# Kernel optimization log

Hardware: AMD Instinct MI355X
Metric: run time of the kernel (lower is better)

The kernel has to match this reference:

```python
import jax, jax.numpy as jnp
import numpy as np

EPS = 1e-5  # PyTorch BatchNorm2d default eps


def _batchnorm(x, gamma, beta):
    # training-mode BN over (N, T, V) per channel; x: [N, C, T, V]
    mean = jnp.mean(x, axis=(0, 2, 3), keepdims=True)
    var = jnp.var(x, axis=(0, 2, 3), keepdims=True)
    inv = jax.lax.rsqrt(var + EPS)
    return (x - mean) * inv * gamma[None, :, None, None] + beta[None, :, None, None]


def setup_inputs() -> dict:
    key = jax.random.key(0)
    ks = jax.random.split(key, 8)
    N, Cin, Cout, T, V, S = 64, 64, 128, 300, 25, 3
    x = jax.random.normal(ks[0], (N, Cin, T, V), dtype=jnp.float32)
    A = jax.random.uniform(ks[1], (S, V, V), dtype=jnp.float32)
    # per-subset 1x1 conv weights/biases (kaiming-ish scale)
    W = jax.random.normal(ks[2], (S, Cout, Cin), dtype=jnp.float32) / np.sqrt(Cin)
    b = jax.random.normal(ks[3], (S, Cout), dtype=jnp.float32) * 0.01
    alpha = jnp.zeros((1,), dtype=jnp.float32)
    bn_gamma = jnp.ones((Cout,), dtype=jnp.float32)
    bn_beta = jnp.zeros((Cout,), dtype=jnp.float32)
    # residual down path (in_channels != out_channels): conv1x1 + BN
    down_W = jax.random.normal(ks[4], (Cout, Cin), dtype=jnp.float32) / np.sqrt(Cin)
    down_b = jax.random.normal(ks[5], (Cout,), dtype=jnp.float32) * 0.01
    down_gamma = jnp.ones((Cout,), dtype=jnp.float32)
    down_beta = jnp.zeros((Cout,), dtype=jnp.float32)
    return {
        "x": x, "A": A, "W": W, "b": b, "alpha": alpha,
        "bn_gamma": bn_gamma, "bn_beta": bn_beta,
        "down_W": down_W, "down_b": down_b,
        "down_gamma": down_gamma, "down_beta": down_beta,
    }


def reference(x, A, W, b, alpha, bn_gamma, bn_beta, down_W, down_b, down_gamma, down_beta):
    V = x.shape[-1]
    eye = jnp.eye(V, dtype=x.dtype)
    A_adj = A + alpha[0] * eye[None]  # [S, V, V]
    # sum_s conv1x1_s( x @ A_s ): fuse adjacency matmul, 1x1 conv, subset sum
    y_agg = jnp.einsum('nctv,svw,soc->notw', x, A_adj, W)
    y_agg = y_agg + jnp.sum(b, axis=0)[None, :, None, None]
    y = _batchnorm(y_agg, bn_gamma, bn_beta)
    # residual down: 1x1 conv + BN (in_channels != out_channels)
    res = jnp.einsum('nctv,oc->notv', x, down_W) + down_b[None, :, None, None]
    res = _batchnorm(res, down_gamma, down_beta)
    return jax.nn.relu(y + res)
```

## Files before the change

### kernel.cpp

```cpp
#include <hip/hip_runtime.h>
#include <hip/hip_bf16.h>

#define N_   64
#define CIN  64
#define COUT 128
#define T_   300
#define V_   25
#define S_   3
#define NTV  (N_ * T_ * V_)

#define TS     10
#define NTB    (T_ / TS)
#define NBLK   (N_ * NTB)
#define RED_ROWS   64
#define RED_BLOCKS (NBLK / RED_ROWS)

#define WS_P    0
#define WS_P2   (WS_P + NBLK * 512)
#define WS_COEF (WS_P2 + RED_BLOCKS * 512)
#define WS_WF   (WS_COEF + 512)
#define WS_WSF  (WS_WF + 16384)
#define WS_AF   (WS_WSF + 16384)

typedef __attribute__((ext_vector_type(8))) short short8;
typedef __attribute__((ext_vector_type(4))) float f32x4;

#define LDS_BARRIER() asm volatile("s_waitcnt lgkmcnt(0)\n\ts_barrier" ::: "memory")

__device__ __forceinline__ unsigned short bfbits(float f) {
    union { __hip_bfloat16 h; unsigned short u; } cv;
    cv.h = __float2bfloat16(f);
    return cv.u;
}
__device__ __forceinline__ unsigned int pack2(float lo, float hi) {
    union { __hip_bfloat162 h2; unsigned int u; } cv;
    cv.h2 = __float22bfloat162_rn(float2{lo, hi});
    return cv.u;
}

__device__ __forceinline__ int zoff(int nl, int k) {
    int slot = (k >> 3) ^ (nl & 31);
    return nl * 512 + slot * 16 + (k & 7) * 2;
}

__global__ __launch_bounds__(256) void k_prep(const float* __restrict__ W,
                                              const float* __restrict__ dW,
                                              const float* __restrict__ A,
                                              const float* __restrict__ alpha,
                                              unsigned short* __restrict__ Wf,
                                              unsigned short* __restrict__ Af) {
    int i = blockIdx.x * 256 + threadIdx.x;
    {
        int j = i & 7, lane = (i >> 3) & 63, ks = (i >> 9) & 7;
        int of = (i >> 12) & 1, oh = i >> 13;
        int o = oh * 32 + of * 16 + (lane & 15);
        int k = ks * 32 + (lane >> 4) * 8 + j;
        float wv = (k < 192) ? W[(k >> 6) * (COUT * CIN) + o * CIN + (k & 63)]
                             : dW[o * CIN + (k - 192)];
        Wf[i] = bfbits(wv);
    }
    if (i < 4096) {
        int j = i & 7, lane = (i >> 3) & 63, wf = (i >> 9) & 1, s = i >> 10;
        int v = (lane >> 4) * 8 + j, w = wf * 16 + (lane & 15);
        float av;
        if (s < 3)
            av = (v < V_ && w < V_)
                   ? A[(s * V_ + v) * V_ + w] + ((v == w) ? alpha[0] : 0.f)
                   : 0.f;
        else
            av = (v == w && v < V_) ? 1.f : 0.f;
        Af[i] = bfbits(av);
    }
}

__global__ __launch_bounds__(256) void k_prep2(const float* __restrict__ W,
                                               const float* __restrict__ dW,
                                               const float* __restrict__ coef,
                                               unsigned short* __restrict__ Wsf) {
    int i = blockIdx.x * 256 + threadIdx.x;
    int j = i & 7, lane = (i >> 3) & 63, ks = (i >> 9) & 7;
    int of = (i >> 12) & 1, oh = i >> 13;
    int o = oh * 32 + of * 16 + (lane & 15);
    int k = ks * 32 + (lane >> 4) * 8 + j;
    float wv = (k < 192) ? W[(k >> 6) * (COUT * CIN) + o * CIN + (k & 63)]
                         : dW[o * CIN + (k - 192)];
    float sc = (k < 192) ? coef[o] : coef[COUT + o];
    Wsf[i] = bfbits(wv * sc);
}

struct XRaw { f32x4 a0, a1; float s; };

__device__ __forceinline__ XRaw load_raw(const float* __restrict__ base, int lq) {
    XRaw r;
    if (lq < 3) {
        r.a0 = *(const f32x4*)(base + lq * 8);
        r.a1 = *(const f32x4*)(base + lq * 8 + 4);
        r.s = 0.f;
    } else {
        r.s = base[24];
        r.a0 = (f32x4){0.f, 0.f, 0.f, 0.f};
        r.a1 = (f32x4){0.f, 0.f, 0.f, 0.f};
    }
    return r;
}

__device__ __forceinline__ short8 cvt_xfr(const XRaw& x, int lq) {
    union { short8 s8; unsigned int u[4]; } b;
    if (lq < 3) {
        b.u[0] = pack2(x.a0[0], x.a0[1]);
        b.u[1] = pack2(x.a0[2], x.a0[3]);
        b.u[2] = pack2(x.a1[0], x.a1[1]);
        b.u[3] = pack2(x.a1[2], x.a1[3]);
    } else {
        b.u[0] = pack2(x.s, 0.f);
        b.u[1] = 0; b.u[2] = 0; b.u[3] = 0;
    }
    return b.s8;
}

__device__ __forceinline__ void stage(char* zb, const unsigned short* Alds,
                                      short8 xfr, int oh, int lq, int lr, int lane) {
    const f32x4 zero = {0.f, 0.f, 0.f, 0.f};
#pragma unroll
    for (int s = 0; s < 4; ++s)
#pragma unroll
        for (int wf = 0; wf < 2; ++wf) {
            short8 af = *(const short8*)(Alds + ((s * 2 + wf) * 64 + lane) * 8);
            f32x4 d = __builtin_amdgcn_mfma_f32_16x16x32_bf16(xfr, af, zero, 0, 0, 0);
            unsigned long long pk = (unsigned long long)pack2(d[0], d[1])
                                  | ((unsigned long long)pack2(d[2], d[3]) << 32);
            int row = wf * 16 + lr;
            int k = s * 64 + oh * 16 + lq * 4;
            *(unsigned long long*)(zb + zoff(row, k)) = pk;
        }
}

template<bool STATS>
__global__ __launch_bounds__(256, 3) void k_gemm(
    const float* __restrict__ x, const unsigned short* __restrict__ Wf,
    const unsigned short* __restrict__ Af, const float* __restrict__ coef,
    float* __restrict__ P, float* __restrict__ out)
{
    __shared__ __align__(16) unsigned short Zt[2][32 * 256];
    __shared__ __align__(16) unsigned short Alds[8 * 64 * 8];

    const int tid = threadIdx.x;
    const int oh = tid >> 6, lane = tid & 63;
    const int lq = lane >> 4, lr = lane & 15;

    const int bid0 = blockIdx.x;
    const int bid = (bid0 & 7) * (NBLK / 8) + (bid0 >> 3);
    const int n = bid / NTB, tb = bid % NTB;
    const int t0 = tb * TS;

    for (int i = tid; i < 512; i += 256)
        *(short8*)(Alds + i * 8) = *(const short8*)(Af + i * 8);

    short8 wfr[2][8];
#pragma unroll
    for (int of = 0; of < 2; ++of)
#pragma unroll
        for (int ks = 0; ks < 8; ++ks)
            wfr[of][ks] = *(const short8*)(Wf + (((oh * 2 + of) * 8 + ks) * 64 + lane) * 8);

    float c0v[2] = {0.f, 0.f};
    if (!STATS) {
        c0v[0] = coef[2 * COUT + oh * 32 + lr];
        c0v[1] = coef[2 * COUT + oh * 32 + 16 + lr];
    }

    float sy[2] = {0.f, 0.f}, sy2[2] = {0.f, 0.f};
    float sr[2] = {0.f, 0.f}, sr2[2] = {0.f, 0.f};

    const int c = oh * 16 + lr;
    const float* xrow = x + ((size_t)(n * CIN + c) * T_) * V_;

    LDS_BARRIER();

    {
        XRaw r0 = load_raw(xrow + (size_t)t0 * V_, lq);
        stage((char*)Zt[0], Alds, cvt_xfr(r0, lq), oh, lq, lr, lane);
    }
    XRaw slotA = load_raw(xrow + (size_t)(t0 + 1) * V_, lq);

    const f32x4 zero = {0.f, 0.f, 0.f, 0.f};

    for (int tt = 0; tt < TS; ++tt) {
        const int t = t0 + tt;
        char* zb = (char*)Zt[tt & 1];
        LDS_BARRIER();

        XRaw slotB;
        if (tt + 2 < TS) slotB = load_raw(xrow + (size_t)(t + 2) * V_, lq);
        else { slotB.a0 = zero; slotB.a1 = zero; slotB.s = 0.f; }

        if (tt + 1 < TS)
            stage((char*)Zt[(tt + 1) & 1], Alds, cvt_xfr(slotA, lq), oh, lq, lr, lane);

        f32x4 acc[2][2];

        if constexpr (STATS) {
#pragma unroll
            for (int ks = 6; ks < 8; ++ks) {
                short8 za[2];
                za[0] = *(const short8*)(zb + zoff(lr, ks * 32 + lq * 8));
                za[1] = *(const short8*)(zb + zoff(16 + lr, ks * 32 + lq * 8));
#pragma unroll
                for (int mf = 0; mf < 2; ++mf)
#pragma unroll
                    for (int of = 0; of < 2; ++of)
                        acc[mf][of] = __builtin_amdgcn_mfma_f32_16x16x32_bf16(
                            za[mf], wfr[of][ks], ks == 6 ? zero : acc[mf][of], 0, 0, 0);
            }
#pragma unroll
            for (int of = 0; of < 2; ++of)
#pragma unroll
                for (int mf = 0; mf < 2; ++mf)
#pragma unroll
                    for (int r = 0; r < 4; ++r) {
                        float rv = acc[mf][of][r];
                        sr[of] += rv; sr2[of] = fmaf(rv, rv, sr2[of]);
                    }
#pragma unroll
            for (int ks = 0; ks < 6; ++ks) {
                short8 za[2];
                za[0] = *(const short8*)(zb + zoff(lr, ks * 32 + lq * 8));
                za[1] = *(const short8*)(zb + zoff(16 + lr, ks * 32 + lq * 8));
#pragma unroll
                for (int mf = 0; mf < 2; ++mf)
#pragma unroll
                    for (int of = 0; of < 2; ++of)
                        acc[mf][of] = __builtin_amdgcn_mfma_f32_16x16x32_bf16(
                            za[mf], wfr[of][ks], ks == 0 ? zero : acc[mf][of], 0, 0, 0);
            }
#pragma unroll
            for (int of = 0; of < 2; ++of)
#pragma unroll
                for (int mf = 0; mf < 2; ++mf)
#pragma unroll
                    for (int r = 0; r < 4; ++r) {
                        float yv = acc[mf][of][r];
                        sy[of] += yv; sy2[of] = fmaf(yv, yv, sy2[of]);
                    }
        } else {
#pragma unroll
            for (int ks = 0; ks < 8; ++ks) {
                short8 za[2];
                za[0] = *(const short8*)(zb + zoff(lr, ks * 32 + lq * 8));
                za[1] = *(const short8*)(zb + zoff(16 + lr, ks * 32 + lq * 8));
#pragma unroll
                for (int mf = 0; mf < 2; ++mf)
#pragma unroll
                    for (int of = 0; of < 2; ++of)
                        acc[mf][of] = __builtin_amdgcn_mfma_f32_16x16x32_bf16(
                            za[mf], wfr[of][ks], ks == 0 ? zero : acc[mf][of], 0, 0, 0);
            }
#pragma unroll
            for (int of = 0; of < 2; ++of) {
                int o = oh * 32 + of * 16 + lr;
                float* rowp = out + ((size_t)(n * COUT + o) * T_ + t) * V_;
                f32x4 v0;
#pragma unroll
                for (int r = 0; r < 4; ++r) v0[r] = fmaxf(acc[0][of][r] + c0v[of], 0.f);
                *(f32x4*)(rowp + lq * 4) = v0;
                if (lq < 2) {
                    f32x4 v1;
#pragma unroll
                    for (int r = 0; r < 4; ++r) v1[r] = fmaxf(acc[1][of][r] + c0v[of], 0.f);
                    *(f32x4*)(rowp + 16 + lq * 4) = v1;
                } else if (lq == 2) {
                    rowp[24] = fmaxf(acc[1][of][0] + c0v[of], 0.f);
                }
            }
        }

        slotA.a0 = slotB.a0; slotA.a1 = slotB.a1; slotA.s = slotB.s;
    }

    if constexpr (STATS) {
#pragma unroll
        for (int of = 0; of < 2; ++of) {
            sy[of]  += __shfl_xor(sy[of], 16);  sy[of]  += __shfl_xor(sy[of], 32);
            sy2[of] += __shfl_xor(sy2[of], 16); sy2[of] += __shfl_xor(sy2[of], 32);
            sr[of]  += __shfl_xor(sr[of], 16);  sr[of]  += __shfl_xor(sr[of], 32);
            sr2[of] += __shfl_xor(sr2[of], 16); sr2[of] += __shfl_xor(sr2[of], 32);
        }
        if (lq == 0) {
            float* p = P + (size_t)bid * 512;
#pragma unroll
            for (int of = 0; of < 2; ++of) {
                int o = oh * 32 + of * 16 + lr;
                p[o] = sy[of]; p[128 + o] = sy2[of];
                p[256 + o] = sr[of]; p[384 + o] = sr2[of];
            }
        }
    }
}

__global__ __launch_bounds__(256) void k_red(const float* __restrict__ P,
                                             float* __restrict__ P2) {
    const int tid = threadIdx.x;
    float a0 = 0.f, a1 = 0.f;
    const int row0 = blockIdx.x * RED_ROWS;
    for (int r = 0; r < RED_ROWS; ++r) {
        const float* p = P + (size_t)(row0 + r) * 512;
        a0 += p[tid];
        a1 += p[256 + tid];
    }
    P2[blockIdx.x * 512 + tid] = a0;
    P2[blockIdx.x * 512 + 256 + tid] = a1;
}

__global__ __launch_bounds__(128) void k_coef(
    const float* __restrict__ P2, const float* __restrict__ gamma,
    const float* __restrict__ beta, const float* __restrict__ dgamma,
    const float* __restrict__ dbeta, const float* __restrict__ b,
    const float* __restrict__ db, float* __restrict__ coef) {
    const int o = threadIdx.x;
    float sy = 0.f, sy2 = 0.f, sr = 0.f, sr2 = 0.f;
    for (int r2 = 0; r2 < RED_BLOCKS; ++r2) {
        const float* p = P2 + r2 * 512;
        sy += p[o]; sy2 += p[128 + o]; sr += p[256 + o]; sr2 += p[384 + o];
    }
    const float bsum = b[o] + b[COUT + o] + b[2 * COUT + o];
    const float dbo = db[o];
    float syb  = sy + (float)NTV * bsum;
    float sy2b = sy2 + 2.f * bsum * sy + (float)NTV * bsum * bsum;
    float srb  = sr + (float)NTV * dbo;
    float sr2b = sr2 + 2.f * dbo * sr + (float)NTV * dbo * dbo;
    const float invn = 1.f / (float)NTV;
    float my = syb * invn, mr = srb * invn;
    float vy = fmaf(-my, my, sy2b * invn);
    float vr = fmaf(-mr, mr, sr2b * invn);
    float ay = rsqrtf(vy + 1e-5f) * gamma[o];
    float ar = rsqrtf(vr + 1e-5f) * dgamma[o];
    float c0 = beta[o] - my * ay + dbeta[o] - mr * ar + ay * bsum + ar * dbo;
    coef[o] = ay; coef[COUT + o] = ar; coef[2 * COUT + o] = c0;
}

extern "C" void kernel_launch(void* const* d_in, const int* in_sizes, int n_in,
                              void* d_out, int out_size, void* d_ws, size_t ws_size,
                              hipStream_t stream) {
    const float* x      = (const float*)d_in[0];
    const float* A      = (const float*)d_in[1];
    const float* W      = (const float*)d_in[2];
    const float* b      = (const float*)d_in[3];
    const float* alpha  = (const float*)d_in[4];
    const float* gamma  = (const float*)d_in[5];
    const float* beta   = (const float*)d_in[6];
    const float* dW     = (const float*)d_in[7];
    const float* db     = (const float*)d_in[8];
    const float* dgamma = (const float*)d_in[9];
    const float* dbeta  = (const float*)d_in[10];

    float* ws   = (float*)d_ws;
    float* P    = ws + WS_P;
    float* P2   = ws + WS_P2;
    float* coef = ws + WS_COEF;
    unsigned short* Wf  = (unsigned short*)(ws + WS_WF);
    unsigned short* Wsf = (unsigned short*)(ws + WS_WSF);
    unsigned short* Af  = (unsigned short*)(ws + WS_AF);
    float* out  = (float*)d_out;

    k_prep<<<128, 256, 0, stream>>>(W, dW, A, alpha, Wf, Af);
    k_gemm<true><<<NBLK, 256, 0, stream>>>(x, Wf, Af, nullptr, P, nullptr);
    k_red<<<RED_BLOCKS, 256, 0, stream>>>(P, P2);
    k_coef<<<1, 128, 0, stream>>>(P2, gamma, beta, dgamma, dbeta, b, db, coef);
    k_prep2<<<128, 256, 0, stream>>>(W, dW, coef, Wsf);
    k_gemm<false><<<NBLK, 256, 0, stream>>>(x, Wsf, Af, coef, nullptr, out);
}
```

Measured before the change: 221.9 us.

## Cache pre-BN conv outputs in bf16 workspace instead of recomputing second GEMM pass

The stats pass now also writes the aggregated and residual conv outputs as bf16 into a padded workspace buffer. A new elementwise finalize kernel then reads them back, applies the BN affine coefficients and ReLU, and writes the output. This replaces the second full GEMM pass, which reloaded x and recomputed the MFMA work. In exchange it adds a large intermediate write and read of about two bf16 tensors the size of the output. That path runs only when the workspace is large enough.

```diff
diff --git a/kernel.cpp b/kernel.cpp
--- a/kernel.cpp
+++ b/kernel.cpp
@@ -15,12 +15,18 @@
 #define RED_ROWS   64
 #define RED_BLOCKS (NBLK / RED_ROWS)
 
+#define YR_ROWB 64
+
 #define WS_P    0
 #define WS_P2   (WS_P + NBLK * 512)
 #define WS_COEF (WS_P2 + RED_BLOCKS * 512)
 #define WS_WF   (WS_COEF + 512)
 #define WS_WSF  (WS_WF + 16384)
 #define WS_AF   (WS_WSF + 16384)
+#define WS_YB   1040000
+#define YFLOATS (NBLK * TS * 128 * YR_ROWB / 4)
+#define WS_RB   (WS_YB + YFLOATS)
+#define WS_END  (WS_RB + YFLOATS)
 
 typedef __attribute__((ext_vector_type(8))) short short8;
 typedef __attribute__((ext_vector_type(4))) float f32x4;
@@ -36,6 +42,9 @@
     union { __hip_bfloat162 h2; unsigned int u; } cv;
     cv.h2 = __float22bfloat162_rn(float2{lo, hi});
     return cv.u;
+}
+__device__ __forceinline__ float bfu(unsigned int low16) {
+    union { float f; unsigned int u; } v; v.u = low16 << 16; return v.f;
 }
 
 __device__ __forceinline__ int zoff(int nl, int k) {
@@ -135,11 +144,20 @@
         }
 }
 
-template<bool STATS>
+__device__ __forceinline__ void yr_store(char* row, int mf, int lq, const f32x4& a) {
+    unsigned long long pk = (unsigned long long)pack2(a[0], a[1])
+                          | ((unsigned long long)pack2(a[2], a[3]) << 32);
+    if (mf == 0)          *(unsigned long long*)(row + lq * 8) = pk;
+    else if (lq < 2)      *(unsigned long long*)(row + 32 + lq * 8) = pk;
+    else if (lq == 2)     *(unsigned long long*)(row + 48) = pk;
+}
+
+template<bool STATS, bool STORE>
 __global__ __launch_bounds__(256, 3) void k_gemm(
     const float* __restrict__ x, const unsigned short* __restrict__ Wf,
     const unsigned short* __restrict__ Af, const float* __restrict__ coef,
-    float* __restrict__ P, float* __restrict__ out)
+    float* __restrict__ P, float* __restrict__ out,
+    unsigned short* __restrict__ Yb, unsigned short* __restrict__ Rb)
 {
     __shared__ __align__(16) unsigned short Zt[2][32 * 256];
     __shared__ __align__(16) unsigned short Alds[8 * 64 * 8];
@@ -175,6 +193,17 @@
     const int c = oh * 16 + lr;
     const float* xrow = x + ((size_t)(n * CIN + c) * T_) * V_;
 
+    char* ybase[2] = {nullptr, nullptr};
+    char* rbase[2] = {nullptr, nullptr};
+    if constexpr (STORE) {
+#pragma unroll
+        for (int of = 0; of < 2; ++of) {
+            size_t off = ((size_t)bid * TS * 128 + oh * 32 + of * 16 + lr) * YR_ROWB;
+            ybase[of] = (char*)Yb + off;
+            rbase[of] = (char*)Rb + off;
+        }
+    }
+
     LDS_BARRIER();
 
     {
@@ -215,12 +244,15 @@
 #pragma unroll
             for (int of = 0; of < 2; ++of)
 #pragma unroll
-                for (int mf = 0; mf < 2; ++mf)
+                for (int mf = 0; mf < 2; ++mf) {
 #pragma unroll
                     for (int r = 0; r < 4; ++r) {
                         float rv = acc[mf][of][r];
                         sr[of] += rv; sr2[of] = fmaf(rv, rv, sr2[of]);
                     }
+                    if constexpr (STORE)
+                        yr_store(rbase[of] + (size_t)tt * (128 * YR_ROWB), mf, lq, acc[mf][of]);
+                }
 #pragma unroll
             for (int ks = 0; ks < 6; ++ks) {
                 short8 za[2];
@@ -236,12 +268,15 @@
 #pragma unroll
             for (int of = 0; of < 2; ++of)
 #pragma unroll
-                for (int mf = 0; mf < 2; ++mf)
+                for (int mf = 0; mf < 2; ++mf) {
 #pragma unroll
                     for (int r = 0; r < 4; ++r) {
                         float yv = acc[mf][of][r];
                         sy[of] += yv; sy2[of] = fmaf(yv, yv, sy2[of]);
                     }
+                    if constexpr (STORE)
+                        yr_store(ybase[of] + (size_t)tt * (128 * YR_ROWB), mf, lq, acc[mf][of]);
+                }
         } else {
 #pragma unroll
             for (int ks = 0; ks < 8; ++ks) {
@@ -292,6 +327,72 @@
                 int o = oh * 32 + of * 16 + lr;
                 p[o] = sy[of]; p[128 + o] = sy2[of];
                 p[256 + o] = sr[of]; p[384 + o] = sr2[of];
+            }
+        }
+    }
+}
+
+__global__ __launch_bounds__(256) void k_fin2(
+    const unsigned short* __restrict__ Yb, const unsigned short* __restrict__ Rb,
+    const float* __restrict__ coef, float* __restrict__ out)
+{
+    const int tid = threadIdx.x;
+    const int oh = tid >> 6, lane = tid & 63;
+    const int lq = lane >> 4, lr = lane & 15;
+
+    const int bid0 = blockIdx.x;
+    const int bid = (bid0 & 7) * (NBLK / 8) + (bid0 >> 3);
+    const int n = bid / NTB, tb = bid % NTB;
+    const int t0 = tb * TS;
+
+    float ayv[2], arv[2], c0v[2];
+#pragma unroll
+    for (int of = 0; of < 2; ++of) {
+        int o = oh * 32 + of * 16 + lr;
+        ayv[of] = coef[o]; arv[of] = coef[COUT + o]; c0v[of] = coef[2 * COUT + o];
+    }
+
+    const char* yb0 = (const char*)Yb + (size_t)bid * TS * 128 * YR_ROWB;
+    const char* rb0 = (const char*)Rb + (size_t)bid * TS * 128 * YR_ROWB;
+
+    for (int tt = 0; tt < TS; ++tt) {
+        const int t = t0 + tt;
+#pragma unroll
+        for (int of = 0; of < 2; ++of) {
+            const int o = oh * 32 + of * 16 + lr;
+            const char* yr = yb0 + (size_t)tt * (128 * YR_ROWB) + o * YR_ROWB;
+            const char* rr = rb0 + (size_t)tt * (128 * YR_ROWB) + o * YR_ROWB;
+            const float ay = ayv[of], ar = arv[of], c0 = c0v[of];
+            float* rowp = out + ((size_t)(n * COUT + o) * T_ + t) * V_;
+
+            unsigned long long yu = *(const unsigned long long*)(yr + lq * 8);
+            unsigned long long ru = *(const unsigned long long*)(rr + lq * 8);
+            f32x4 v;
+#pragma unroll
+            for (int r = 0; r < 4; ++r) {
+                float yf = bfu((unsigned int)(yu >> (16 * r)) & 0xffffu);
+                float rf = bfu((unsigned int)(ru >> (16 * r)) & 0xffffu);
+                v[r] = fmaxf(fmaf(ay, yf, fmaf(ar, rf, c0)), 0.f);
+            }
+            *(f32x4*)(rowp + lq * 4) = v;
+
+            if (lq < 2) {
+                unsigned long long yu1 = *(const unsigned long long*)(yr + 32 + lq * 8);
+                unsigned long long ru1 = *(const unsigned long long*)(rr + 32 + lq * 8);
+                f32x4 v1;
+#pragma unroll
+                for (int r = 0; r < 4; ++r) {
+                    float yf = bfu((unsigned int)(yu1 >> (16 * r)) & 0xffffu);
+                    float rf = bfu((unsigned int)(ru1 >> (16 * r)) & 0xffffu);
+                    v1[r] = fmaxf(fmaf(ay, yf, fmaf(ar, rf, c0)), 0.f);
+                }
+                *(f32x4*)(rowp + 16 + lq * 4) = v1;
+            } else if (lq == 2) {
+                unsigned int yu2 = *(const unsigned int*)(yr + 48);
+                unsigned int ru2 = *(const unsigned int*)(rr + 48);
+                float yf = bfu(yu2 & 0xffffu);
+                float rf = bfu(ru2 & 0xffffu);
+                rowp[24] = fmaxf(fmaf(ay, yf, fmaf(ar, rf, c0)), 0.f);
             }
         }
     }
@@ -362,10 +463,21 @@
     unsigned short* Af  = (unsigned short*)(ws + WS_AF);
     float* out  = (float*)d_out;
 
+    const bool big = ws_size >= (size_t)WS_END * sizeof(float);
+
     k_prep<<<128, 256, 0, stream>>>(W, dW, A, alpha, Wf, Af);
-    k_gemm<true><<<NBLK, 256, 0, stream>>>(x, Wf, Af, nullptr, P, nullptr);
-    k_red<<<RED_BLOCKS, 256, 0, stream>>>(P, P2);
-    k_coef<<<1, 128, 0, stream>>>(P2, gamma, beta, dgamma, dbeta, b, db, coef);
-    k_prep2<<<128, 256, 0, stream>>>(W, dW, coef, Wsf);
-    k_gemm<false><<<NBLK, 256, 0, stream>>>(x, Wsf, Af, coef, nullptr, out);
-}
+    if (big) {
+        unsigned short* Yb = (unsigned short*)(ws + WS_YB);
+        unsigned short* Rb = (unsigned short*)(ws + WS_RB);
+        k_gemm<true, true><<<NBLK, 256, 0, stream>>>(x, Wf, Af, nullptr, P, nullptr, Yb, Rb);
+        k_red<<<RED_BLOCKS, 256, 0, stream>>>(P, P2);
+        k_coef<<<1, 128, 0, stream>>>(P2, gamma, beta, dgamma, dbeta, b, db, coef);
+        k_fin2<<<NBLK, 256, 0, stream>>>(Yb, Rb, coef, out);
+    } else {
+        k_gemm<true, false><<<NBLK, 256, 0, stream>>>(x, Wf, Af, nullptr, P, nullptr, nullptr, nullptr);
+        k_red<<<RED_BLOCKS, 256, 0, stream>>>(P, P2);
+        k_coef<<<1, 128, 0, stream>>>(P2, gamma, beta, dgamma, dbeta, b, db, coef);
+        k_prep2<<<128, 256, 0, stream>>>(W, dW, coef, Wsf);
+        k_gemm<false, false><<<NBLK, 256, 0, stream>>>(x, Wsf, Af, coef, nullptr, out, nullptr, nullptr);
+    }
+}
```

Result: slower. 460.2 us (+107.4%).

## Make each wave stage its own full Z tile to remove block barriers

Applied to the files above, without the earlier changes.

Each wave now loads all 64 input channels (four channel quarters) and computes the full adjacency-aggregated Z tile into a private LDS buffer. That removes the per-timestep block-wide barriers and the shared double buffer. Z fragments are read into registers before the next step's tile is staged into the same buffer. The cost is four times the staging MFMA and x-load work per wave, more registers and LDS, and occupancy lowered from 3 to 2 blocks per SM.

```diff
diff --git a/kernel.cpp b/kernel.cpp
--- a/kernel.cpp
+++ b/kernel.cpp
@@ -14,6 +14,7 @@
 #define NBLK   (N_ * NTB)
 #define RED_ROWS   64
 #define RED_BLOCKS (NBLK / RED_ROWS)
+#define QOFF   (16 * T_ * V_)
 
 #define WS_P    0
 #define WS_P2   (WS_P + NBLK * 512)
@@ -24,8 +25,6 @@
 
 typedef __attribute__((ext_vector_type(8))) short short8;
 typedef __attribute__((ext_vector_type(4))) float f32x4;
-
-#define LDS_BARRIER() asm volatile("s_waitcnt lgkmcnt(0)\n\ts_barrier" ::: "memory")
 
 __device__ __forceinline__ unsigned short bfbits(float f) {
     union { __hip_bfloat16 h; unsigned short u; } cv;
@@ -118,30 +117,33 @@
     return b.s8;
 }
 
-__device__ __forceinline__ void stage(char* zb, const unsigned short* Alds,
-                                      short8 xfr, int oh, int lq, int lr, int lane) {
+__device__ __forceinline__ void stage_full(char* zw, const unsigned short* Alds,
+                                           const short8* xf, int lq, int lr, int lane) {
     const f32x4 zero = {0.f, 0.f, 0.f, 0.f};
 #pragma unroll
     for (int s = 0; s < 4; ++s)
 #pragma unroll
         for (int wf = 0; wf < 2; ++wf) {
             short8 af = *(const short8*)(Alds + ((s * 2 + wf) * 64 + lane) * 8);
-            f32x4 d = __builtin_amdgcn_mfma_f32_16x16x32_bf16(xfr, af, zero, 0, 0, 0);
-            unsigned long long pk = (unsigned long long)pack2(d[0], d[1])
-                                  | ((unsigned long long)pack2(d[2], d[3]) << 32);
-            int row = wf * 16 + lr;
-            int k = s * 64 + oh * 16 + lq * 4;
-            *(unsigned long long*)(zb + zoff(row, k)) = pk;
+#pragma unroll
+            for (int cq = 0; cq < 4; ++cq) {
+                f32x4 d = __builtin_amdgcn_mfma_f32_16x16x32_bf16(xf[cq], af, zero, 0, 0, 0);
+                unsigned long long pk = (unsigned long long)pack2(d[0], d[1])
+                                      | ((unsigned long long)pack2(d[2], d[3]) << 32);
+                int row = wf * 16 + lr;
+                int k = s * 64 + cq * 16 + lq * 4;
+                *(unsigned long long*)(zw + zoff(row, k)) = pk;
+            }
         }
 }
 
 template<bool STATS>
-__global__ __launch_bounds__(256, 3) void k_gemm(
+__global__ __launch_bounds__(256, 2) void k_gemm(
     const float* __restrict__ x, const unsigned short* __restrict__ Wf,
     const unsigned short* __restrict__ Af, const float* __restrict__ coef,
     float* __restrict__ P, float* __restrict__ out)
 {
-    __shared__ __align__(16) unsigned short Zt[2][32 * 256];
+    __shared__ __align__(16) unsigned short Zt[4][32 * 256];
     __shared__ __align__(16) unsigned short Alds[8 * 64 * 8];
 
     const int tid = threadIdx.x;
@@ -172,46 +174,50 @@
     float sy[2] = {0.f, 0.f}, sy2[2] = {0.f, 0.f};
     float sr[2] = {0.f, 0.f}, sr2[2] = {0.f, 0.f};
 
-    const int c = oh * 16 + lr;
-    const float* xrow = x + ((size_t)(n * CIN + c) * T_) * V_;
-
-    LDS_BARRIER();
-
+    const float* xrow = x + ((size_t)(n * CIN + lr) * T_) * V_;
+    char* zw = (char*)Zt[oh];
+
+    __syncthreads();
+
+    short8 xf[4];
     {
-        XRaw r0 = load_raw(xrow + (size_t)t0 * V_, lq);
-        stage((char*)Zt[0], Alds, cvt_xfr(r0, lq), oh, lq, lr, lane);
-    }
-    XRaw slotA = load_raw(xrow + (size_t)(t0 + 1) * V_, lq);
+        XRaw r4[4];
+#pragma unroll
+        for (int cq = 0; cq < 4; ++cq)
+            r4[cq] = load_raw(xrow + cq * QOFF + (size_t)t0 * V_, lq);
+#pragma unroll
+        for (int cq = 0; cq < 4; ++cq) xf[cq] = cvt_xfr(r4[cq], lq);
+        stage_full(zw, Alds, xf, lq, lr, lane);
+    }
+    XRaw slot[4];
+#pragma unroll
+    for (int cq = 0; cq < 4; ++cq)
+        slot[cq] = load_raw(xrow + cq * QOFF + (size_t)(t0 + 1) * V_, lq);
 
     const f32x4 zero = {0.f, 0.f, 0.f, 0.f};
 
     for (int tt = 0; tt < TS; ++tt) {
         const int t = t0 + tt;
-        char* zb = (char*)Zt[tt & 1];
-        LDS_BARRIER();
-
-        XRaw slotB;
-        if (tt + 2 < TS) slotB = load_raw(xrow + (size_t)(t + 2) * V_, lq);
-        else { slotB.a0 = zero; slotB.a1 = zero; slotB.s = 0.f; }
-
-        if (tt + 1 < TS)
-            stage((char*)Zt[(tt + 1) & 1], Alds, cvt_xfr(slotA, lq), oh, lq, lr, lane);
+
+        short8 za0[8], za1[8];
+#pragma unroll
+        for (int ks = 0; ks < 8; ++ks) {
+            za0[ks] = *(const short8*)(zw + zoff(lr, ks * 32 + lq * 8));
+            za1[ks] = *(const short8*)(zw + zoff(16 + lr, ks * 32 + lq * 8));
+        }
 
         f32x4 acc[2][2];
 
         if constexpr (STATS) {
 #pragma unroll
-            for (int ks = 6; ks < 8; ++ks) {
-                short8 za[2];
-                za[0] = *(const short8*)(zb + zoff(lr, ks * 32 + lq * 8));
-                za[1] = *(const short8*)(zb + zoff(16 + lr, ks * 32 + lq * 8));
-#pragma unroll
-                for (int mf = 0; mf < 2; ++mf)
-#pragma unroll
-                    for (int of = 0; of < 2; ++of)
-                        acc[mf][of] = __builtin_amdgcn_mfma_f32_16x16x32_bf16(
-                            za[mf], wfr[of][ks], ks == 6 ? zero : acc[mf][of], 0, 0, 0);
-            }
+            for (int ks = 6; ks < 8; ++ks)
+#pragma unroll
+                for (int of = 0; of < 2; ++of) {
+                    acc[0][of] = __builtin_amdgcn_mfma_f32_16x16x32_bf16(
+                        za0[ks], wfr[of][ks], ks == 6 ? zero : acc[0][of], 0, 0, 0);
+                    acc[1][of] = __builtin_amdgcn_mfma_f32_16x16x32_bf16(
+                        za1[ks], wfr[of][ks], ks == 6 ? zero : acc[1][of], 0, 0, 0);
+                }
 #pragma unroll
             for (int of = 0; of < 2; ++of)
 #pragma unroll
@@ -222,16 +228,22 @@
                         sr[of] += rv; sr2[of] = fmaf(rv, rv, sr2[of]);
                     }
 #pragma unroll
-            for (int ks = 0; ks < 6; ++ks) {
-                short8 za[2];
-                za[0] = *(const short8*)(zb + zoff(lr, ks * 32 + lq * 8));
-                za[1] = *(const short8*)(zb + zoff(16 + lr, ks * 32 + lq * 8));
-#pragma unroll
-                for (int mf = 0; mf < 2; ++mf)
-#pragma unroll
-                    for (int of = 0; of < 2; ++of)
-                        acc[mf][of] = __builtin_amdgcn_mfma_f32_16x16x32_bf16(
-                            za[mf], wfr[of][ks], ks == 0 ? zero : acc[mf][of], 0, 0, 0);
+            for (int ks = 0; ks < 6; ++ks)
+#pragma unroll
+                for (int of = 0; of < 2; ++of) {
+                    acc[0][of] = __builtin_amdgcn_mfma_f32_16x16x32_bf16(
+                        za0[ks], wfr[of][ks], ks == 0 ? zero : acc[0][of], 0, 0, 0);
+                    acc[1][of] = __builtin_amdgcn_mfma_f32_16x16x32_bf16(
+                        za1[ks], wfr[of][ks], ks == 0 ? zero : acc[1][of], 0, 0, 0);
+                }
+            if (tt + 1 < TS) {
+#pragma unroll
+                for (int cq = 0; cq < 4; ++cq) xf[cq] = cvt_xfr(slot[cq], lq);
+                if (tt + 2 < TS)
+#pragma unroll
+                    for (int cq = 0; cq < 4; ++cq)
+                        slot[cq] = load_raw(xrow + cq * QOFF + (size_t)(t + 2) * V_, lq);
+                stage_full(zw, Alds, xf, lq, lr, lane);
             }
 #pragma unroll
             for (int of = 0; of < 2; ++of)
@@ -244,16 +256,22 @@
                     }
         } else {
 #pragma unroll
-            for (int ks = 0; ks < 8; ++ks) {
-                short8 za[2];
-                za[0] = *(const short8*)(zb + zoff(lr, ks * 32 + lq * 8));
-                za[1] = *(const short8*)(zb + zoff(16 + lr, ks * 32 + lq * 8));
-#pragma unroll
-                for (int mf = 0; mf < 2; ++mf)
-#pragma unroll
-                    for (int of = 0; of < 2; ++of)
-                        acc[mf][of] = __builtin_amdgcn_mfma_f32_16x16x32_bf16(
-                            za[mf], wfr[of][ks], ks == 0 ? zero : acc[mf][of], 0, 0, 0);
+            for (int ks = 0; ks < 8; ++ks)
+#pragma unroll
+                for (int of = 0; of < 2; ++of) {
+                    acc[0][of] = __builtin_amdgcn_mfma_f32_16x16x32_bf16(
+                        za0[ks], wfr[of][ks], ks == 0 ? zero : acc[0][of], 0, 0, 0);
+                    acc[1][of] = __builtin_amdgcn_mfma_f32_16x16x32_bf16(
+                        za1[ks], wfr[of][ks], ks == 0 ? zero : acc[1][of], 0, 0, 0);
+                }
+            if (tt + 1 < TS) {
+#pragma unroll
+                for (int cq = 0; cq < 4; ++cq) xf[cq] = cvt_xfr(slot[cq], lq);
+                if (tt + 2 < TS)
+#pragma unroll
+                    for (int cq = 0; cq < 4; ++cq)
+                        slot[cq] = load_raw(xrow + cq * QOFF + (size_t)(t + 2) * V_, lq);
+                stage_full(zw, Alds, xf, lq, lr, lane);
             }
 #pragma unroll
             for (int of = 0; of < 2; ++of) {
@@ -273,8 +291,6 @@
                 }
             }
         }
-
-        slotA.a0 = slotB.a0; slotA.a1 = slotB.a1; slotA.s = slotB.s;
     }
 
     if constexpr (STATS) {
```

Result: slower. 403.0 us (+81.6%).
